# Performance work log

Measured on AMD Instinct MI355X. Metric: run time of the kernel, lower is better.

Reference implementation:

```python
import jax, jax.numpy as jnp
import numpy as np

N_NODES = 50000
N_EDGES = 600000


def gcn_conv(x, src, dst, W, b, num_nodes):
    # x: [N, Cin] -> [N, Cout]; symmetric-normalized GCN with self-loops
    h = x @ W  # [N, Cout]
    loop = jnp.arange(num_nodes, dtype=src.dtype)
    s = jnp.concatenate([src, loop])
    d = jnp.concatenate([dst, loop])
    ones = jnp.ones(s.shape[0], dtype=h.dtype)
    deg = jax.ops.segment_sum(ones, d, num_segments=num_nodes)  # in-degree incl self-loop
    dinv = jnp.where(deg > 0, jax.lax.rsqrt(deg), 0.0)
    norm = dinv[s] * dinv[d]  # [E+N]
    msg = h[s] * norm[:, None]  # gather + scale
    out = jax.ops.segment_sum(msg, d, num_segments=num_nodes)  # scatter-add
    return out + b


def setup_inputs() -> dict:
    key = jax.random.key(0)
    k1, k2, k3, k4 = jax.random.split(key, 4)
    x = jax.random.normal(k1, (N_NODES, 128), dtype=jnp.float32)
    edge_index = jax.random.randint(k2, (2, N_EDGES), 0, N_NODES, dtype=jnp.int64)
    W1 = jax.random.normal(k3, (128, 128), dtype=jnp.float32) * (1.0 / np.sqrt(128))
    b1 = jnp.zeros((128,), dtype=jnp.float32)
    W2 = jax.random.normal(k4, (128, 64), dtype=jnp.float32) * (1.0 / np.sqrt(128))
    b2 = jnp.zeros((64,), dtype=jnp.float32)
    return {"x": x, "edge_index": edge_index, "W1": W1, "b1": b1, "W2": W2, "b2": b2}


def reference(x, edge_index, W1, b1, W2, b2):
    src, dst = edge_index[0], edge_index[1]
    h = gcn_conv(x, src, dst, W1, b1, N_NODES)
    h = jax.nn.relu(h)
    out = gcn_conv(h, src, dst, W2, b2, N_NODES)
    return out
```

## Files before the change

kernel.cpp:

```cpp
#include <hip/hip_runtime.h>
#include <cstddef>
#include <cstdint>

#define N_NODES 50000
#define N_EDGES 600000
#define M_TILES 3125
#define GEMM_BLKS 782
#define NBUCK 196
#define BUCK_CAP 4096
#define K1_BLKS 147
#define K1_EDGES 4096

typedef short bf16x8 __attribute__((ext_vector_type(8)));
typedef float f32x4 __attribute__((ext_vector_type(4)));


__device__ __forceinline__ unsigned short f32_to_bf16(float x) {
  unsigned u = __float_as_uint(x);
  u += 0x7FFFu + ((u >> 16) & 1u);
  return (unsigned short)(u >> 16);
}
__device__ __forceinline__ float bf16_to_f32(unsigned short h) {
  return __uint_as_float((unsigned)h << 16);
}
__device__ __forceinline__ float bf16_lo(unsigned g) {
  return __uint_as_float(g << 16);
}
__device__ __forceinline__ float bf16_hi(unsigned g) {
  return __uint_as_float(g & 0xFFFF0000u);
}

__device__ __forceinline__ void split8(const float* __restrict__ p, bf16x8& hi,
                                       bf16x8& lo) {
  const float4 v0 = *(const float4*)p;
  const float4 v1 = *(const float4*)(p + 4);
  float v[8] = {v0.x, v0.y, v0.z, v0.w, v1.x, v1.y, v1.z, v1.w};
#pragma unroll
  for (int i = 0; i < 8; i++) {
    const unsigned short h = f32_to_bf16(v[i]);
    hi[i] = (short)h;
    lo[i] = (short)f32_to_bf16(v[i] - bf16_to_f32(h));
  }
}

__global__ __launch_bounds__(256) void k_prep(
    const float* __restrict__ W1, const float* __restrict__ W2,
    unsigned short* __restrict__ w1h, unsigned short* __restrict__ w1l,
    unsigned short* __restrict__ w2h, unsigned short* __restrict__ w2l,
    int* __restrict__ cursor) {
  const int b = blockIdx.x;
  const int tid = threadIdx.x;
  if (b < 96) {
    const int i = b * 256 + tid;
    const float* W;
    unsigned short *wh, *wl;
    int o, cout;
    if (i < 16384) {
      W = W1; wh = w1h; wl = w1l; o = i; cout = 128;
    } else {
      W = W2; wh = w2h; wl = w2l; o = i - 16384; cout = 64;
    }
    const int j = o & 7;
    const int lane = (o >> 3) & 63;
    const int t = o >> 9;
    const int ks = t & 3;
    const int ct = t >> 2;
    const int k = ks * 32 + (lane >> 4) * 8 + j;
    const int n = ct * 16 + (lane & 15);
    const float v = W[k * cout + n];
    const unsigned short h = f32_to_bf16(v);
    wh[o] = h;
    wl[o] = f32_to_bf16(v - bf16_to_f32(h));
  } else {
    if (tid < NBUCK) cursor[tid] = tid * BUCK_CAP;
  }
}

template <int COUT>
__device__ __forceinline__ void gemm_body(const int wtile, const int lane,
                                          const float* __restrict__ X,
                                          const unsigned short* __restrict__ Wph,
                                          const unsigned short* __restrict__ Wpl,
                                          unsigned short* __restrict__ Hs) {
  constexpr int CT = COUT / 16;
  const int m = lane & 15;
  const int q = lane >> 4;

  f32x4 acc[CT];
#pragma unroll
  for (int ct = 0; ct < CT; ct++) acc[ct] = {0.f, 0.f, 0.f, 0.f};

  const float* xp = X + (size_t)(wtile * 16 + m) * 128 + q * 8;

#pragma unroll
  for (int ks = 0; ks < 4; ks++) {
    bf16x8 ah, al;
    split8(xp + ks * 32, ah, al);
#pragma unroll
    for (int ct = 0; ct < CT; ct++) {
      const size_t bo = ((size_t)(ct * 4 + ks) * 64 + lane) * 8;
      const bf16x8 bh = *(const bf16x8*)(Wph + bo);
      const bf16x8 bl = *(const bf16x8*)(Wpl + bo);
      acc[ct] = __builtin_amdgcn_mfma_f32_16x16x32_bf16(ah, bh, acc[ct], 0, 0, 0);
      acc[ct] = __builtin_amdgcn_mfma_f32_16x16x32_bf16(al, bh, acc[ct], 0, 0, 0);
      acc[ct] = __builtin_amdgcn_mfma_f32_16x16x32_bf16(ah, bl, acc[ct], 0, 0, 0);
    }
  }
#pragma unroll
  for (int ct = 0; ct < CT; ct++) {
#pragma unroll
    for (int r = 0; r < 4; r++) {
      const int orow = wtile * 16 + q * 4 + r;
      Hs[(size_t)orow * COUT + ct * 16 + m] = f32_to_bf16(acc[ct][r]);
    }
  }
}

__global__ __launch_bounds__(256) void k_route_gemm128(
    const float* __restrict__ X, const unsigned short* __restrict__ Wph,
    const unsigned short* __restrict__ Wpl, unsigned short* __restrict__ Hs,
    const int* __restrict__ src, const int* __restrict__ dst,
    int* __restrict__ cursor, unsigned* __restrict__ routed) {
  __shared__ int hist[NBUCK];
  __shared__ int lcur[NBUCK];
  const int tid = threadIdx.x;
  if (blockIdx.x < K1_BLKS) {
    for (int t = tid; t < NBUCK; t += 256) hist[t] = 0;
    __syncthreads();
    unsigned packed[16];
    bool cvalid[4];
    const int base = blockIdx.x * K1_EDGES;
#pragma unroll
    for (int c = 0; c < 4; c++) {
      const int i4 = base + c * 1024 + tid * 4;
      cvalid[c] = (i4 < N_EDGES);
      if (cvalid[c]) {
        const int4 d4 = *(const int4*)(dst + i4);
        const int4 s4 = *(const int4*)(src + i4);
        packed[c * 4 + 0] = ((unsigned)d4.x << 16) | (unsigned)s4.x;
        packed[c * 4 + 1] = ((unsigned)d4.y << 16) | (unsigned)s4.y;
        packed[c * 4 + 2] = ((unsigned)d4.z << 16) | (unsigned)s4.z;
        packed[c * 4 + 3] = ((unsigned)d4.w << 16) | (unsigned)s4.w;
#pragma unroll
        for (int j = 0; j < 4; j++)
          atomicAdd(&hist[packed[c * 4 + j] >> 24], 1);
      }
    }
    __syncthreads();
    for (int t = tid; t < NBUCK; t += 256)
      lcur[t] = atomicAdd(&cursor[t], hist[t]);
    __syncthreads();
#pragma unroll
    for (int c = 0; c < 4; c++) {
      if (cvalid[c]) {
#pragma unroll
        for (int j = 0; j < 4; j++) {
          const unsigned pk = packed[c * 4 + j];
          const int slot = atomicAdd(&lcur[pk >> 24], 1);
          routed[slot] = pk;
        }
      }
    }
  } else {
    const int wtile = (blockIdx.x - K1_BLKS) * 4 + (tid >> 6);
    if (wtile < M_TILES) gemm_body<128>(wtile, tid & 63, X, Wph, Wpl, Hs);
  }
}

__global__ __launch_bounds__(1024) void k_bsort(
    const unsigned* __restrict__ routed, const int* __restrict__ cursor,
    int* __restrict__ counts, int* __restrict__ start,
    int* __restrict__ sorted_src) {
  __shared__ unsigned ebuf[BUCK_CAP];
  __shared__ int h2[256];
  __shared__ int c2[256];
  const int b = blockIdx.x;
  const int tid = threadIdx.x;
  const int n = cursor[b] - b * BUCK_CAP;
  for (int i = tid; i < n; i += 1024) ebuf[i] = routed[b * BUCK_CAP + i];
  if (tid < 256) h2[tid] = 0;
  __syncthreads();
  for (int i = tid; i < n; i += 1024)
    atomicAdd(&h2[(ebuf[i] >> 16) & 255], 1);
  __syncthreads();
  int own = 0;
  if (tid < 256) own = h2[tid];
  for (int s = 1; s < 256; s <<= 1) {
    int t = 0;
    if (tid < 256 && tid >= s) t = h2[tid - s];
    __syncthreads();
    if (tid < 256) h2[tid] += t;
    __syncthreads();
  }
  if (tid < 256) {
    const int pfx = h2[tid] - own;
    c2[tid] = pfx;
    const int d = b * 256 + tid;
    if (d < N_NODES) {
      counts[d] = own;
      start[d] = b * BUCK_CAP + pfx;
    }
  }
  __syncthreads();
  for (int i = tid; i < n; i += 1024) {
    const unsigned pk = ebuf[i];
    const int r = atomicAdd(&c2[(pk >> 16) & 255], 1);
    sorted_src[b * BUCK_CAP + r] = (int)(pk & 0xFFFFu);
  }
}

__global__ __launch_bounds__(256) void k_agg128_gemm64(
    const unsigned* __restrict__ Hb, const int* __restrict__ counts,
    const int* __restrict__ start, const int* __restrict__ sorted_src,
    const float* __restrict__ bias, const unsigned short* __restrict__ Wph,
    const unsigned short* __restrict__ Wpl, unsigned short* __restrict__ Hs) {
  __shared__ float a1s[16][132];
  const int lane = threadIdx.x & 63;
  const int wave = threadIdx.x >> 6;
  const float2 bb = ((const float2*)bias)[lane];

  int deg[4], e0v[4];
  float dvv[4];
  unsigned gselfv[4];
  int siv[4];
  float wiv[4];
#pragma unroll
  for (int i = 0; i < 4; i++) {
    const int v = blockIdx.x * 16 + wave * 4 + i;
    deg[i] = counts[v];
    e0v[i] = start[v];
  }
#pragma unroll
  for (int i = 0; i < 4; i++) {
    const int v = blockIdx.x * 16 + wave * 4 + i;
    dvv[i] = rsqrtf((float)deg[i] + 1.0f);
    gselfv[i] = Hb[(size_t)v * 64 + lane];
    siv[i] = (lane < deg[i]) ? sorted_src[e0v[i] + lane] : 0;
  }
#pragma unroll
  for (int i = 0; i < 4; i++) {
    wiv[i] = (lane < deg[i]) ? rsqrtf((float)counts[siv[i]] + 1.0f) * dvv[i]
                             : 0.f;
  }

#pragma unroll
  for (int i = 0; i < 4; i++) {
    const int r = wave * 4 + i;
    const float dv = dvv[i];
    float ax = bf16_lo(gselfv[i]) * (dv * dv);
    float ay = bf16_hi(gselfv[i]) * (dv * dv);
    const int dg = min(deg[i], 64);

    int j = 0;
    for (; j + 8 <= dg; j += 8) {
      int s[8];
      float w[8];
      unsigned g[8];
#pragma unroll
      for (int t = 0; t < 8; t++) {
        s[t] = __shfl(siv[i], j + t);
        w[t] = __shfl(wiv[i], j + t);
      }
#pragma unroll
      for (int t = 0; t < 8; t++) g[t] = Hb[(size_t)s[t] * 64 + lane];
#pragma unroll
      for (int t = 0; t < 8; t++) {
        ax += bf16_lo(g[t]) * w[t];
        ay += bf16_hi(g[t]) * w[t];
      }
    }
    for (; j + 4 <= dg; j += 4) {
      int s[4];
      float w[4];
      unsigned g[4];
#pragma unroll
      for (int t = 0; t < 4; t++) {
        s[t] = __shfl(siv[i], j + t);
        w[t] = __shfl(wiv[i], j + t);
      }
#pragma unroll
      for (int t = 0; t < 4; t++) g[t] = Hb[(size_t)s[t] * 64 + lane];
#pragma unroll
      for (int t = 0; t < 4; t++) {
        ax += bf16_lo(g[t]) * w[t];
        ay += bf16_hi(g[t]) * w[t];
      }
    }
    for (; j < dg; j++) {
      const int s = __shfl(siv[i], j);
      const float w = __shfl(wiv[i], j);
      const unsigned g = Hb[(size_t)s * 64 + lane];
      ax += bf16_lo(g) * w;
      ay += bf16_hi(g) * w;
    }
    a1s[r][lane * 2] = fmaxf(ax + bb.x, 0.f);
    a1s[r][lane * 2 + 1] = fmaxf(ay + bb.y, 0.f);
  }
  __syncthreads();

  const int ct = wave;
  const int m = lane & 15;
  const int q = lane >> 4;
  f32x4 acc = {0.f, 0.f, 0.f, 0.f};
#pragma unroll
  for (int ks = 0; ks < 4; ks++) {
    bf16x8 ah, al;
    split8(&a1s[m][ks * 32 + q * 8], ah, al);
    const size_t bo = ((size_t)(ct * 4 + ks) * 64 + lane) * 8;
    const bf16x8 bh = *(const bf16x8*)(Wph + bo);
    const bf16x8 bl = *(const bf16x8*)(Wpl + bo);
    acc = __builtin_amdgcn_mfma_f32_16x16x32_bf16(ah, bh, acc, 0, 0, 0);
    acc = __builtin_amdgcn_mfma_f32_16x16x32_bf16(al, bh, acc, 0, 0, 0);
    acc = __builtin_amdgcn_mfma_f32_16x16x32_bf16(ah, bl, acc, 0, 0, 0);
  }
#pragma unroll
  for (int r = 0; r < 4; r++) {
    const int orow = blockIdx.x * 16 + q * 4 + r;
    Hs[(size_t)orow * 64 + ct * 16 + m] = f32_to_bf16(acc[r]);
  }
}

__global__ __launch_bounds__(256) void k_agg64(
    const unsigned* __restrict__ Hb, const int* __restrict__ counts,
    const int* __restrict__ start, const int* __restrict__ sorted_src,
    const float* __restrict__ bias, float* __restrict__ out) {
  const int hl = threadIdx.x & 31;
  const int v = blockIdx.x * 8 + (threadIdx.x >> 5);
  if (v >= N_NODES) return;
  const int deg = counts[v];
  const float dv = rsqrtf((float)deg + 1.0f);
  const int e0 = start[v];

  const unsigned gself = Hb[(size_t)v * 32 + hl];
  float ax = bf16_lo(gself) * (dv * dv);
  float ay = bf16_hi(gself) * (dv * dv);

  for (int base = 0; base < deg; base += 32) {
    const int cnt = min(32, deg - base);
    int si = 0;
    float wi = 0.f;
    if (base + hl < deg) {
      si = sorted_src[e0 + base + hl];
      wi = rsqrtf((float)counts[si] + 1.0f) * dv;
    }
    int j = 0;
    for (; j + 8 <= cnt; j += 8) {
      int s[8];
      float w[8];
      unsigned g[8];
#pragma unroll
      for (int t = 0; t < 8; t++) {
        s[t] = __shfl(si, j + t, 32);
        w[t] = __shfl(wi, j + t, 32);
      }
#pragma unroll
      for (int t = 0; t < 8; t++) g[t] = Hb[(size_t)s[t] * 32 + hl];
#pragma unroll
      for (int t = 0; t < 8; t++) {
        ax += bf16_lo(g[t]) * w[t];
        ay += bf16_hi(g[t]) * w[t];
      }
    }
    for (; j + 4 <= cnt; j += 4) {
      int s[4];
      float w[4];
      unsigned g[4];
#pragma unroll
      for (int t = 0; t < 4; t++) {
        s[t] = __shfl(si, j + t, 32);
        w[t] = __shfl(wi, j + t, 32);
      }
#pragma unroll
      for (int t = 0; t < 4; t++) g[t] = Hb[(size_t)s[t] * 32 + hl];
#pragma unroll
      for (int t = 0; t < 4; t++) {
        ax += bf16_lo(g[t]) * w[t];
        ay += bf16_hi(g[t]) * w[t];
      }
    }
    for (; j < cnt; j++) {
      const int s = __shfl(si, j, 32);
      const float w = __shfl(wi, j, 32);
      const unsigned g = Hb[(size_t)s * 32 + hl];
      ax += bf16_lo(g) * w;
      ay += bf16_hi(g) * w;
    }
  }
  const float2 b = ((const float2*)bias)[hl];
  float2 r;
  r.x = ax + b.x;
  r.y = ay + b.y;
  ((float2*)out)[(size_t)v * 32 + hl] = r;
}


extern "C" void kernel_launch(void* const* d_in, const int* in_sizes, int n_in,
                              void* d_out, int out_size, void* d_ws, size_t ws_size,
                              hipStream_t stream) {
  const float* x = (const float*)d_in[0];
  const int* ei = (const int*)d_in[1];
  const float* W1 = (const float*)d_in[2];
  const float* b1 = (const float*)d_in[3];
  const float* W2 = (const float*)d_in[4];
  const float* b2 = (const float*)d_in[5];
  const int* src = ei;
  const int* dst = ei + N_EDGES;

  char* p = (char*)d_ws;
  auto alloc = [&](size_t bytes) {
    char* q = p;
    p += (bytes + 255) & ~(size_t)255;
    return q;
  };
  int* cursor = (int*)alloc((size_t)NBUCK * 4);
  unsigned* routed = (unsigned*)alloc((size_t)NBUCK * BUCK_CAP * 4);
  int* sorted_src = (int*)alloc((size_t)NBUCK * BUCK_CAP * 4);
  int* counts = (int*)alloc((size_t)N_NODES * 4);
  int* start = (int*)alloc((size_t)N_NODES * 4);
  unsigned short* w1h = (unsigned short*)alloc(16384 * 2);
  unsigned short* w1l = (unsigned short*)alloc(16384 * 2);
  unsigned short* w2h = (unsigned short*)alloc(8192 * 2);
  unsigned short* w2l = (unsigned short*)alloc(8192 * 2);
  unsigned short* h1b = (unsigned short*)alloc((size_t)N_NODES * 128 * 2);
  unsigned short* h2b = (unsigned short*)alloc((size_t)N_NODES * 64 * 2);

  hipLaunchKernelGGL(k_prep, dim3(97), dim3(256), 0, stream, W1, W2, w1h, w1l,
                     w2h, w2l, cursor);
  hipLaunchKernelGGL(k_route_gemm128, dim3(K1_BLKS + GEMM_BLKS), dim3(256), 0,
                     stream, x, w1h, w1l, h1b, src, dst, cursor, routed);
  hipLaunchKernelGGL(k_bsort, dim3(NBUCK), dim3(1024), 0, stream, routed,
                     cursor, counts, start, sorted_src);
  hipLaunchKernelGGL(k_agg128_gemm64, dim3(M_TILES), dim3(256), 0, stream,
                     (const unsigned*)h1b, counts, start, sorted_src, b1, w2h,
                     w2l, h2b);
  hipLaunchKernelGGL(k_agg64, dim3((N_NODES + 7) / 8), dim3(256), 0, stream,
                     (const unsigned*)h2b, counts, start, sorted_src, b2,
                     (float*)d_out);
}
```

Before: 152.2 us.

## Route edges into per-block slots and fuse first GEMM with bucket sort

Edge routing moves into the weight-prep kernel. Each block writes into fixed per-(bucket, block) slots of capacity 64, with per-block counts stored separately, which removes the global cursor atomics and the cursor-init step. The bucket sort now compacts these slots with a wave prefix scan, and the first-layer GEMM runs as extra blocks of that same kernel, cutting one launch and overlapping the GEMM with the sort. The risk is that the fixed capacity of 64 edges per bucket per block could overflow on skewed degree distributions.

```diff
diff --git a/kernel.cpp b/kernel.cpp
--- a/kernel.cpp
+++ b/kernel.cpp
@@ -5,11 +5,12 @@
 #define N_NODES 50000
 #define N_EDGES 600000
 #define M_TILES 3125
-#define GEMM_BLKS 782
 #define NBUCK 196
 #define BUCK_CAP 4096
-#define K1_BLKS 147
+#define ROUTE_BLKS 147
 #define K1_EDGES 4096
+#define CAPB 64
+#define GEMM16_BLKS 196
 
 typedef short bf16x8 __attribute__((ext_vector_type(8)));
 typedef float f32x4 __attribute__((ext_vector_type(4)));
@@ -43,11 +44,62 @@
   }
 }
 
-__global__ __launch_bounds__(256) void k_prep(
+__device__ __forceinline__ int wave_incl_scan(int v, int lane) {
+#pragma unroll
+  for (int d = 1; d < 64; d <<= 1) {
+    int t = __shfl_up(v, d, 64);
+    if (lane >= d) v += t;
+  }
+  return v;
+}
+
+template <int COUT>
+__device__ __forceinline__ void gemm_body(const int wtile, const int lane,
+                                          const float* __restrict__ X,
+                                          const unsigned short* __restrict__ Wph,
+                                          const unsigned short* __restrict__ Wpl,
+                                          unsigned short* __restrict__ Hs) {
+  constexpr int CT = COUT / 16;
+  const int m = lane & 15;
+  const int q = lane >> 4;
+
+  f32x4 acc[CT];
+#pragma unroll
+  for (int ct = 0; ct < CT; ct++) acc[ct] = {0.f, 0.f, 0.f, 0.f};
+
+  const float* xp = X + (size_t)(wtile * 16 + m) * 128 + q * 8;
+
+#pragma unroll
+  for (int ks = 0; ks < 4; ks++) {
+    bf16x8 ah, al;
+    split8(xp + ks * 32, ah, al);
+#pragma unroll
+    for (int ct = 0; ct < CT; ct++) {
+      const size_t bo = ((size_t)(ct * 4 + ks) * 64 + lane) * 8;
+      const bf16x8 bh = *(const bf16x8*)(Wph + bo);
+      const bf16x8 bl = *(const bf16x8*)(Wpl + bo);
+      acc[ct] = __builtin_amdgcn_mfma_f32_16x16x32_bf16(ah, bh, acc[ct], 0, 0, 0);
+      acc[ct] = __builtin_amdgcn_mfma_f32_16x16x32_bf16(al, bh, acc[ct], 0, 0, 0);
+      acc[ct] = __builtin_amdgcn_mfma_f32_16x16x32_bf16(ah, bl, acc[ct], 0, 0, 0);
+    }
+  }
+#pragma unroll
+  for (int ct = 0; ct < CT; ct++) {
+#pragma unroll
+    for (int r = 0; r < 4; r++) {
+      const int orow = wtile * 16 + q * 4 + r;
+      Hs[(size_t)orow * COUT + ct * 16 + m] = f32_to_bf16(acc[ct][r]);
+    }
+  }
+}
+
+__global__ __launch_bounds__(256) void k_prep_route(
     const float* __restrict__ W1, const float* __restrict__ W2,
     unsigned short* __restrict__ w1h, unsigned short* __restrict__ w1l,
     unsigned short* __restrict__ w2h, unsigned short* __restrict__ w2l,
-    int* __restrict__ cursor) {
+    const int* __restrict__ src, const int* __restrict__ dst,
+    unsigned* __restrict__ routed, int* __restrict__ cnt) {
+  __shared__ int lcnt[NBUCK];
   const int b = blockIdx.x;
   const int tid = threadIdx.x;
   if (b < 96) {
@@ -72,116 +124,80 @@
     wh[o] = h;
     wl[o] = f32_to_bf16(v - bf16_to_f32(h));
   } else {
-    if (tid < NBUCK) cursor[tid] = tid * BUCK_CAP;
-  }
-}
-
-template <int COUT>
-__device__ __forceinline__ void gemm_body(const int wtile, const int lane,
-                                          const float* __restrict__ X,
-                                          const unsigned short* __restrict__ Wph,
-                                          const unsigned short* __restrict__ Wpl,
-                                          unsigned short* __restrict__ Hs) {
-  constexpr int CT = COUT / 16;
-  const int m = lane & 15;
-  const int q = lane >> 4;
-
-  f32x4 acc[CT];
-#pragma unroll
-  for (int ct = 0; ct < CT; ct++) acc[ct] = {0.f, 0.f, 0.f, 0.f};
-
-  const float* xp = X + (size_t)(wtile * 16 + m) * 128 + q * 8;
-
-#pragma unroll
-  for (int ks = 0; ks < 4; ks++) {
-    bf16x8 ah, al;
-    split8(xp + ks * 32, ah, al);
-#pragma unroll
-    for (int ct = 0; ct < CT; ct++) {
-      const size_t bo = ((size_t)(ct * 4 + ks) * 64 + lane) * 8;
-      const bf16x8 bh = *(const bf16x8*)(Wph + bo);
-      const bf16x8 bl = *(const bf16x8*)(Wpl + bo);
-      acc[ct] = __builtin_amdgcn_mfma_f32_16x16x32_bf16(ah, bh, acc[ct], 0, 0, 0);
-      acc[ct] = __builtin_amdgcn_mfma_f32_16x16x32_bf16(al, bh, acc[ct], 0, 0, 0);
-      acc[ct] = __builtin_amdgcn_mfma_f32_16x16x32_bf16(ah, bl, acc[ct], 0, 0, 0);
-    }
-  }
-#pragma unroll
-  for (int ct = 0; ct < CT; ct++) {
-#pragma unroll
-    for (int r = 0; r < 4; r++) {
-      const int orow = wtile * 16 + q * 4 + r;
-      Hs[(size_t)orow * COUT + ct * 16 + m] = f32_to_bf16(acc[ct][r]);
-    }
-  }
-}
-
-__global__ __launch_bounds__(256) void k_route_gemm128(
-    const float* __restrict__ X, const unsigned short* __restrict__ Wph,
-    const unsigned short* __restrict__ Wpl, unsigned short* __restrict__ Hs,
-    const int* __restrict__ src, const int* __restrict__ dst,
-    int* __restrict__ cursor, unsigned* __restrict__ routed) {
-  __shared__ int hist[NBUCK];
-  __shared__ int lcur[NBUCK];
-  const int tid = threadIdx.x;
-  if (blockIdx.x < K1_BLKS) {
-    for (int t = tid; t < NBUCK; t += 256) hist[t] = 0;
+    const int r = b - 96;
+    for (int t = tid; t < NBUCK; t += 256) lcnt[t] = 0;
     __syncthreads();
-    unsigned packed[16];
-    bool cvalid[4];
-    const int base = blockIdx.x * K1_EDGES;
+    const int base = r * K1_EDGES;
 #pragma unroll
     for (int c = 0; c < 4; c++) {
       const int i4 = base + c * 1024 + tid * 4;
-      cvalid[c] = (i4 < N_EDGES);
-      if (cvalid[c]) {
+      if (i4 < N_EDGES) {
         const int4 d4 = *(const int4*)(dst + i4);
         const int4 s4 = *(const int4*)(src + i4);
-        packed[c * 4 + 0] = ((unsigned)d4.x << 16) | (unsigned)s4.x;
-        packed[c * 4 + 1] = ((unsigned)d4.y << 16) | (unsigned)s4.y;
-        packed[c * 4 + 2] = ((unsigned)d4.z << 16) | (unsigned)s4.z;
-        packed[c * 4 + 3] = ((unsigned)d4.w << 16) | (unsigned)s4.w;
-#pragma unroll
-        for (int j = 0; j < 4; j++)
-          atomicAdd(&hist[packed[c * 4 + j] >> 24], 1);
+        unsigned pk[4];
+        pk[0] = ((unsigned)d4.x << 16) | (unsigned)s4.x;
+        pk[1] = ((unsigned)d4.y << 16) | (unsigned)s4.y;
+        pk[2] = ((unsigned)d4.z << 16) | (unsigned)s4.z;
+        pk[3] = ((unsigned)d4.w << 16) | (unsigned)s4.w;
+#pragma unroll
+        for (int j = 0; j < 4; j++) {
+          const int bk = pk[j] >> 24;
+          const int pos = atomicAdd(&lcnt[bk], 1);
+          routed[((size_t)bk * ROUTE_BLKS + r) * CAPB + pos] = pk[j];
+        }
       }
     }
     __syncthreads();
-    for (int t = tid; t < NBUCK; t += 256)
-      lcur[t] = atomicAdd(&cursor[t], hist[t]);
-    __syncthreads();
-#pragma unroll
-    for (int c = 0; c < 4; c++) {
-      if (cvalid[c]) {
-#pragma unroll
-        for (int j = 0; j < 4; j++) {
-          const unsigned pk = packed[c * 4 + j];
-          const int slot = atomicAdd(&lcur[pk >> 24], 1);
-          routed[slot] = pk;
-        }
-      }
-    }
-  } else {
-    const int wtile = (blockIdx.x - K1_BLKS) * 4 + (tid >> 6);
-    if (wtile < M_TILES) gemm_body<128>(wtile, tid & 63, X, Wph, Wpl, Hs);
-  }
-}
-
-__global__ __launch_bounds__(1024) void k_bsort(
-    const unsigned* __restrict__ routed, const int* __restrict__ cursor,
+    for (int t = tid; t < NBUCK; t += 256) cnt[t * ROUTE_BLKS + r] = lcnt[t];
+  }
+}
+
+__global__ __launch_bounds__(1024) void k_bsort_gemm128(
+    const unsigned* __restrict__ routed, const int* __restrict__ cnt,
     int* __restrict__ counts, int* __restrict__ start,
-    int* __restrict__ sorted_src) {
+    int* __restrict__ sorted_src, const float* __restrict__ X,
+    const unsigned short* __restrict__ Wph,
+    const unsigned short* __restrict__ Wpl, unsigned short* __restrict__ Hs) {
   __shared__ unsigned ebuf[BUCK_CAP];
+  __shared__ int scnt[ROUTE_BLKS];
+  __shared__ int soff[ROUTE_BLKS];
   __shared__ int h2[256];
   __shared__ int c2[256];
+  const int tid = threadIdx.x;
+  const int lane = tid & 63;
+  const int wave = tid >> 6;
+
+  if (blockIdx.x >= NBUCK) {
+    const int wtile = (blockIdx.x - NBUCK) * 16 + wave;
+    if (wtile < M_TILES) gemm_body<128>(wtile, lane, X, Wph, Wpl, Hs);
+    return;
+  }
+
   const int b = blockIdx.x;
-  const int tid = threadIdx.x;
-  const int n = cursor[b] - b * BUCK_CAP;
-  for (int i = tid; i < n; i += 1024) ebuf[i] = routed[b * BUCK_CAP + i];
+  if (tid < ROUTE_BLKS) scnt[tid] = cnt[b * ROUTE_BLKS + tid];
+  __syncthreads();
+  if (wave == 0) {
+    int carry = 0;
+#pragma unroll
+    for (int c = 0; c < 3; c++) {
+      const int idx = c * 64 + lane;
+      const int v = (idx < ROUTE_BLKS) ? scnt[idx] : 0;
+      const int inc = wave_incl_scan(v, lane);
+      if (idx < ROUTE_BLKS) soff[idx] = carry + inc - v;
+      carry += __shfl(inc, 63);
+    }
+  }
+  __syncthreads();
+  for (int k = wave; k < ROUTE_BLKS; k += 16) {
+    const int len = scnt[k];
+    if (lane < len)
+      ebuf[soff[k] + lane] =
+          routed[((size_t)b * ROUTE_BLKS + k) * CAPB + lane];
+  }
+  const int n = soff[ROUTE_BLKS - 1] + scnt[ROUTE_BLKS - 1];
   if (tid < 256) h2[tid] = 0;
   __syncthreads();
-  for (int i = tid; i < n; i += 1024)
-    atomicAdd(&h2[(ebuf[i] >> 16) & 255], 1);
+  for (int i = tid; i < n; i += 1024) atomicAdd(&h2[(ebuf[i] >> 16) & 255], 1);
   __syncthreads();
   int own = 0;
   if (tid < 256) own = h2[tid];
@@ -336,7 +352,7 @@
   float ay = bf16_hi(gself) * (dv * dv);
 
   for (int base = 0; base < deg; base += 32) {
-    const int cnt = min(32, deg - base);
+    const int cnt2 = min(32, deg - base);
     int si = 0;
     float wi = 0.f;
     if (base + hl < deg) {
@@ -344,7 +360,7 @@
       wi = rsqrtf((float)counts[si] + 1.0f) * dv;
     }
     int j = 0;
-    for (; j + 8 <= cnt; j += 8) {
+    for (; j + 8 <= cnt2; j += 8) {
       int s[8];
       float w[8];
       unsigned g[8];
@@ -361,7 +377,7 @@
         ay += bf16_hi(g[t]) * w[t];
       }
     }
-    for (; j + 4 <= cnt; j += 4) {
+    for (; j + 4 <= cnt2; j += 4) {
       int s[4];
       float w[4];
       unsigned g[4];
@@ -378,7 +394,7 @@
         ay += bf16_hi(g[t]) * w[t];
       }
     }
-    for (; j < cnt; j++) {
+    for (; j < cnt2; j++) {
       const int s = __shfl(si, j, 32);
       const float w = __shfl(wi, j, 32);
       const unsigned g = Hb[(size_t)s * 32 + hl];
@@ -412,8 +428,8 @@
     p += (bytes + 255) & ~(size_t)255;
     return q;
   };
-  int* cursor = (int*)alloc((size_t)NBUCK * 4);
-  unsigned* routed = (unsigned*)alloc((size_t)NBUCK * BUCK_CAP * 4);
+  unsigned* routed = (unsigned*)alloc((size_t)NBUCK * ROUTE_BLKS * CAPB * 4);
+  int* cnt = (int*)alloc((size_t)NBUCK * ROUTE_BLKS * 4);
   int* sorted_src = (int*)alloc((size_t)NBUCK * BUCK_CAP * 4);
   int* counts = (int*)alloc((size_t)N_NODES * 4);
   int* start = (int*)alloc((size_t)N_NODES * 4);
@@ -424,12 +440,11 @@
   unsigned short* h1b = (unsigned short*)alloc((size_t)N_NODES * 128 * 2);
   unsigned short* h2b = (unsigned short*)alloc((size_t)N_NODES * 64 * 2);
 
-  hipLaunchKernelGGL(k_prep, dim3(97), dim3(256), 0, stream, W1, W2, w1h, w1l,
-                     w2h, w2l, cursor);
-  hipLaunchKernelGGL(k_route_gemm128, dim3(K1_BLKS + GEMM_BLKS), dim3(256), 0,
-                     stream, x, w1h, w1l, h1b, src, dst, cursor, routed);
-  hipLaunchKernelGGL(k_bsort, dim3(NBUCK), dim3(1024), 0, stream, routed,
-                     cursor, counts, start, sorted_src);
+  hipLaunchKernelGGL(k_prep_route, dim3(96 + ROUTE_BLKS), dim3(256), 0, stream,
+                     W1, W2, w1h, w1l, w2h, w2l, src, dst, routed, cnt);
+  hipLaunchKernelGGL(k_bsort_gemm128, dim3(NBUCK + GEMM16_BLKS), dim3(1024), 0,
+                     stream, routed, cnt, counts, start, sorted_src, x, w1h,
+                     w1l, h1b);
   hipLaunchKernelGGL(k_agg128_gemm64, dim3(M_TILES), dim3(256), 0, stream,
                      (const unsigned*)h1b, counts, start, sorted_src, b1, w2h,
                      w2l, h2b);
```

Result: no change. 155.2 us (+1.9%).
